# Kernel tuning notes

Hardware: AMD Instinct MI355X
Metric: run time of the kernel (lower is better)

The kernel has to match this reference:

```python
import jax, jax.numpy as jnp
import numpy as np

NUM_HEADS = 32
NUM_KV_HEADS = 8
HEAD_DIM = 128
HIDDEN = 4096
BASE = 10000.0


def setup_inputs() -> dict:
    key = jax.random.key(0)
    ks = jax.random.split(key, 9)
    bs, seq = 1, 2048
    x = jax.random.normal(ks[0], (bs, seq, HIDDEN), dtype=jnp.float32)
    position_ids = jnp.broadcast_to(jnp.arange(seq, dtype=jnp.int32), (bs, seq))
    s = 1.0 / np.sqrt(HIDDEN)
    wq = jax.random.normal(ks[1], (NUM_HEADS * HEAD_DIM, HIDDEN), dtype=jnp.float32) * s
    bq = jnp.zeros((NUM_HEADS * HEAD_DIM,), dtype=jnp.float32)
    wk = jax.random.normal(ks[2], (NUM_KV_HEADS * HEAD_DIM, HIDDEN), dtype=jnp.float32) * s
    bk = jnp.zeros((NUM_KV_HEADS * HEAD_DIM,), dtype=jnp.float32)
    wv = jax.random.normal(ks[3], (NUM_KV_HEADS * HEAD_DIM, HIDDEN), dtype=jnp.float32) * s
    bv = jnp.zeros((NUM_KV_HEADS * HEAD_DIM,), dtype=jnp.float32)
    wo = jax.random.normal(ks[4], (HIDDEN, NUM_HEADS * HEAD_DIM), dtype=jnp.float32) * s
    bo = jnp.zeros((HIDDEN,), dtype=jnp.float32)
    return {"x": x, "position_ids": position_ids, "wq": wq, "bq": bq,
            "wk": wk, "bk": bk, "wv": wv, "bv": bv, "wo": wo, "bo": bo}


def _rotate_half(t):
    h = t.shape[-1] // 2
    return jnp.concatenate([-t[..., h:], t[..., :h]], axis=-1)


def _rope_cos_sin(position_ids, dtype):
    # inv_freq: (head_dim/2,)
    inv_freq = 1.0 / (BASE ** (jnp.arange(0, HEAD_DIM, 2, dtype=jnp.float32) / HEAD_DIM))
    freqs = position_ids.astype(jnp.float32)[..., None] * inv_freq  # (bs, seq, hd/2)
    emb = jnp.concatenate([freqs, freqs], axis=-1)  # (bs, seq, hd)
    return jnp.cos(emb).astype(dtype), jnp.sin(emb).astype(dtype)


def reference(x, position_ids, wq, bq, wk, bk, wv, bv, wo, bo):
    bs, seq, _ = x.shape
    g = NUM_HEADS // NUM_KV_HEADS
    # projections -> (bs, heads, seq, head_dim)
    q = (x @ wq.T + bq).reshape(bs, seq, NUM_HEADS, HEAD_DIM).transpose(0, 2, 1, 3)
    k = (x @ wk.T + bk).reshape(bs, seq, NUM_KV_HEADS, HEAD_DIM).transpose(0, 2, 1, 3)
    v = (x @ wv.T + bv).reshape(bs, seq, NUM_KV_HEADS, HEAD_DIM).transpose(0, 2, 1, 3)
    cos, sin = _rope_cos_sin(position_ids, x.dtype)
    cos, sin = cos[:, None], sin[:, None]  # broadcast over heads
    q = q * cos + _rotate_half(q) * sin
    k = k * cos + _rotate_half(k) * sin
    # grouped attention without expanding kv (same math as repeat_kv)
    qg = q.reshape(bs, NUM_KV_HEADS, g, seq, HEAD_DIM)
    scores = jnp.einsum('bhgqd,bhkd->bhgqk', qg, k) / jnp.sqrt(
        jnp.asarray(HEAD_DIM, dtype=jnp.float32)).astype(x.dtype)
    probs = jax.nn.softmax(scores.astype(jnp.float32), axis=-1).astype(x.dtype)
    out = jnp.einsum('bhgqk,bhkd->bhgqd', probs, v)  # (bs, kvh, g, seq, hd)
    out = out.reshape(bs, NUM_HEADS, seq, HEAD_DIM).transpose(0, 2, 1, 3)
    out = out.reshape(bs, seq, NUM_HEADS * HEAD_DIM)
    return out @ wo.T + bo
```

## Files before the change

kernel.cpp:

```cpp
#include <hip/hip_runtime.h>
#include <stdint.h>

typedef unsigned short u16;
typedef unsigned long long u64;
typedef __attribute__((ext_vector_type(8))) short s8v;
typedef __attribute__((ext_vector_type(4))) float f4v;

#define MFMA(a, b, c) __builtin_amdgcn_mfma_f32_16x16x32_bf16((a), (b), (c), 0, 0, 0)

__device__ __forceinline__ u16 f2b(float f) {
  uint32_t x = __float_as_uint(f);
  x += 0x7fff + ((x >> 16) & 1);
  return (u16)(x >> 16);
}
__device__ __forceinline__ float b2f(u16 u) {
  return __uint_as_float(((uint32_t)u) << 16);
}

__device__ __forceinline__ void gll16(const void* g, void* l) {
  __builtin_amdgcn_global_load_lds((const __attribute__((address_space(1))) uint32_t*)g,
                                   (__attribute__((address_space(3))) uint32_t*)l, 16, 0, 0);
}
__device__ __forceinline__ void bar() { __builtin_amdgcn_s_barrier(); }

__global__ void cvt_all(const float* __restrict__ x, const float* __restrict__ wq,
                        const float* __restrict__ wk, const float* __restrict__ wv,
                        const float* __restrict__ wo,
                        u16* __restrict__ xb, u16* __restrict__ wqkv, u16* __restrict__ wob) {
  int i = blockIdx.x * 256 + threadIdx.x;
  const float* s; u16* d; size_t off;
  if      (i < 1048576) { s = x;  d = xb;   off = (size_t)i; }
  else if (i < 3145728) { s = wq; d = wqkv; off = (size_t)(i - 1048576); }
  else if (i < 3670016) { s = wk; d = wqkv + (size_t)16777216; off = (size_t)(i - 3145728); }
  else if (i < 4194304) { s = wv; d = wqkv + (size_t)20971520; off = (size_t)(i - 3670016); }
  else                  { s = wo; d = wob;  off = (size_t)(i - 4194304); }
  const float4* sp = (const float4*)(s + off * 8);
  float4 f0 = sp[0], f1 = sp[1];
  s8v o;
  o[0] = (short)f2b(f0.x); o[1] = (short)f2b(f0.y); o[2] = (short)f2b(f0.z); o[3] = (short)f2b(f0.w);
  o[4] = (short)f2b(f1.x); o[5] = (short)f2b(f1.y); o[6] = (short)f2b(f1.z); o[7] = (short)f2b(f1.w);
  *(s8v*)(d + off * 8) = o;
}

template <int BM, int MODE>
__global__ __launch_bounds__(512, 2) void gemm8p(
    const u16* __restrict__ A, const u16* __restrict__ Bact,
    const float* __restrict__ bias,
    float* __restrict__ Cf, u16* __restrict__ Cq, u16* __restrict__ Ck, u16* __restrict__ Cv,
    int K) {
  extern __shared__ u16 smem[];
  constexpr int AO = BM * 64;
  constexpr int BE = 2 * BM * 64;
  constexpr int BO = BE + 16384;
  constexpr int MI = BM / 64;
  constexpr int NH = BM / 64;

  const int tid = threadIdx.x;
  const int l = tid & 63, wv = tid >> 6;
  const int wm = wv >> 2, wn = wv & 3;
  const int lr = l & 15, lg = l >> 4;
  const int swz = 16 * (lr & 7);
  const int wrow = wm * (BM / 2);

  const int nwg = gridDim.x;
  int bid = blockIdx.x;
  bid = (bid & 7) * (nwg >> 3) + (bid >> 3);
  const int NB = 8;
  const int m0 = (bid / NB) * BM, n0 = (bid % NB) * 256;

  const size_t K64 = (size_t)64 * K;

  const int sr = tid >> 3;
  const int sc = ((tid & 7) ^ (sr & 7)) * 8;
  const u16* gA = A + (size_t)(m0 + sr) * K + sc;
  const u16* gB = Bact + (size_t)(n0 + sr) * K + sc;

  auto STA = [&](int P, int h, int kt) {
    gll16(gA + (size_t)(h * 64) * K + (size_t)kt * 64,
          smem + (P ? AO : 0) + h * 4096 + tid * 8);
  };
  auto STB = [&](int P, int h, int kt) {
    const u16* g = gB + (size_t)(h * 128) * K + (size_t)kt * 64;
    u16* d = smem + (P ? BO : BE) + h * 8192 + tid * 8;
    gll16(g, d);
    gll16(g + K64, d + 4096);
  };

  const char* smc = (const char*)smem;
  s8v a[MI][2], b0[2][2], b1[2][2];
  auto LDA = [&](int P, int QR) {
#pragma unroll
    for (int mi = 0; mi < MI; ++mi)
#pragma unroll
      for (int kk = 0; kk < 2; ++kk)
        a[mi][kk] = *(const s8v*)(smc + (P ? AO * 2 : 0) +
            (wrow + QR * (BM / 4) + mi * 16 + lr) * 128 + ((kk * 64 + lg * 16) ^ swz));
  };
  auto LDB = [&](int P, int QC, s8v bb[2][2]) {
#pragma unroll
    for (int ni = 0; ni < 2; ++ni)
#pragma unroll
      for (int kk = 0; kk < 2; ++kk)
        bb[ni][kk] = *(const s8v*)(smc + (P ? BO * 2 : BE * 2) +
            (wn * 64 + QC * 32 + ni * 16 + lr) * 128 + ((kk * 64 + lg * 16) ^ swz));
  };

  f4v acc[BM / 32][4];
#pragma unroll
  for (int i = 0; i < BM / 32; ++i)
#pragma unroll
    for (int j = 0; j < 4; ++j) acc[i][j] = {0.f, 0.f, 0.f, 0.f};

#define PHMF(QR, QC, B)                                                        \
  __builtin_amdgcn_s_setprio(1);                                               \
  _Pragma("unroll") for (int mi = 0; mi < MI; ++mi)                            \
    _Pragma("unroll") for (int ni = 0; ni < 2; ++ni)                           \
      _Pragma("unroll") for (int kk = 0; kk < 2; ++kk)                         \
        acc[(QR) * MI + mi][(QC) * 2 + ni] =                                   \
            MFMA(a[mi][kk], B[ni][kk], acc[(QR) * MI + mi][(QC) * 2 + ni]);    \
  __builtin_amdgcn_s_setprio(0);

  STB(0, 0, 0); STB(0, 1, 0);
#pragma unroll
  for (int h = 0; h < NH; ++h) STA(0, h, 0);
  STB(1, 0, 1); STB(1, 1, 1);
  asm volatile("s_waitcnt vmcnt(4)" ::: "memory");
  bar();

  const int ITERS = K >> 7;
  for (int i = 0; i < ITERS; ++i) {
    const int kn = 2 * i + 2;
    const bool more = (i + 1 < ITERS);
    LDA(0, 0); LDB(0, 0, b0);
    STA(1, 0, 2 * i + 1);
    bar(); PHMF(0, 0, b0); bar();
    LDB(0, 1, b1);
    STA(1, 1, 2 * i + 1);
    bar(); PHMF(0, 1, b1); bar();
    LDA(0, 1);
    if constexpr (NH > 2) STA(1, 2, 2 * i + 1);
    if (more) STB(0, 0, kn);
    bar(); PHMF(1, 1, b1); bar();
    if (more) STB(0, 1, kn);
    bar(); PHMF(1, 0, b0);
    if (more) asm volatile("s_waitcnt vmcnt(4)" ::: "memory");
    else      asm volatile("s_waitcnt vmcnt(0)" ::: "memory");
    bar();
    LDA(1, 0); LDB(1, 0, b0);
    if (more) STA(0, 0, kn);
    bar(); PHMF(0, 0, b0); bar();
    LDB(1, 1, b1);
    if (more) STA(0, 1, kn);
    bar(); PHMF(0, 1, b1); bar();
    LDA(1, 1);
    if (more) {
      if constexpr (NH > 2) STA(0, 2, kn);
      STB(1, 0, 2 * i + 3);
    }
    bar(); PHMF(1, 1, b1); bar();
    if (more) STB(1, 1, 2 * i + 3);
    bar(); PHMF(1, 0, b0);
    asm volatile("s_waitcnt vmcnt(4)" ::: "memory");
    bar();
  }
#undef PHMF

  bar();

  if constexpr (MODE == 2) {
#pragma unroll
    for (int fi = 0; fi < BM / 32; ++fi) {
      const int f0 = m0 + wrow + fi * 16;
      if (f0 >= 5120) {
#pragma unroll
        for (int fj = 0; fj < 4; ++fj)
#pragma unroll
          for (int r = 0; r < 4; ++r) {
            const int f = f0 + lg * 4 + r;
            const int tok = n0 + wn * 64 + fj * 16 + lr;
            Cv[(size_t)(f - 5120) * 2048 + tok] = f2b(acc[fi][fj][r] + bias[f]);
          }
      }
    }
    if (m0 + wrow < 5120) {
      u16* buf = smem + wv * 3328;
#pragma unroll
      for (int c = 0; c < 2; ++c) {
#pragma unroll
        for (int fj2 = 0; fj2 < 2; ++fj2) {
          const int fj = 2 * c + fj2;
          const int tl = fj2 * 16 + lr;
#pragma unroll
          for (int fi = 0; fi < BM / 32; ++fi) {
            const int f0 = m0 + wrow + fi * 16;
            if (f0 < 5120) {
#pragma unroll
              for (int r = 0; r < 4; ++r) {
                const int fl = fi * 16 + lg * 4 + r;
                buf[tl * 104 + fl] = f2b(acc[fi][fj][r] + bias[m0 + wrow + fl]);
              }
            }
          }
        }
        asm volatile("s_waitcnt lgkmcnt(0)" ::: "memory");
        const int row = l >> 1, half = l & 1;
        const int tok = n0 + wn * 64 + c * 32 + row;
#pragma unroll
        for (int i2 = 0; i2 < 6; ++i2) {
          const int flc = (2 * i2 + half) * 8;
          const int f = m0 + wrow + flc;
          if (f < 4096)
            *(s8v*)(Cq + (size_t)tok * 4096 + f) = *(const s8v*)(buf + row * 104 + flc);
          else if (f < 5120)
            *(s8v*)(Ck + (size_t)tok * 1024 + (f - 4096)) = *(const s8v*)(buf + row * 104 + flc);
        }
        asm volatile("s_waitcnt lgkmcnt(0)" ::: "memory");
      }
    }
  } else {
    float* buf = (float*)smem + wv * 1088;
#pragma unroll
    for (int c = 0; c < 4; ++c) {
#pragma unroll
      for (int fi = 0; fi < BM / 32; ++fi)
#pragma unroll
        for (int r = 0; r < 4; ++r) {
          const int fl = fi * 16 + lg * 4 + r;
          buf[lr * 68 + fl] = acc[fi][c][r] + bias[m0 + wrow + fl];
        }
      asm volatile("s_waitcnt lgkmcnt(0)" ::: "memory");
      const int row = l >> 2, q4 = l & 3;
      const int tok = n0 + wn * 64 + c * 16 + row;
      float* g = Cf + (size_t)tok * 4096 + m0 + wrow + q4 * 16;
      const float* src = buf + row * 68 + q4 * 16;
#pragma unroll
      for (int i2 = 0; i2 < 4; ++i2)
        *(f4v*)(g + i2 * 4) = *(const f4v*)(src + i2 * 4);
      asm volatile("s_waitcnt lgkmcnt(0)" ::: "memory");
    }
  }
}

__global__ void rope_kernel(u16* __restrict__ q, u16* __restrict__ k, const int* __restrict__ pos) {
  int i = blockIdx.x * 256 + threadIdx.x;
  const int NQ = 2048 * 32 * 64;
  const int NK = 2048 * 8 * 64;
  u16* buf;
  int m, d, stride, h;
  if (i < NQ) { buf = q; m = i >> 11; h = (i >> 6) & 31; d = i & 63; stride = 4096; }
  else {
    i -= NQ; if (i >= NK) return;
    buf = k; m = i >> 9; h = (i >> 6) & 7; d = i & 63; stride = 1024;
  }
  size_t base = (size_t)m * stride + h * 128 + d;
  float a = b2f(buf[base]), b = b2f(buf[base + 64]);
  float p = (float)pos[m];
  float ang = p * exp2f(-0.20762050593045952f * (float)d);
  float s, c;
  sincosf(ang, &s, &c);
  buf[base]      = f2b(a * c - b * s);
  buf[base + 64] = f2b(b * c + a * s);
}

__global__ __launch_bounds__(512, 4) void attn_kernel(const u16* __restrict__ Q, const u16* __restrict__ Kb,
                                                      const u16* __restrict__ Vt, u16* __restrict__ Ao) {
  __shared__ __align__(16) u16 Ks[64 * 128];
  __shared__ __align__(16) u16 Vs[128 * 64];
  __shared__ __align__(16) u16 Ps[8][16 * 64];
  const int tid = threadIdx.x;
  const int l = tid & 63, wv = tid >> 6;
  const int lr = l & 15, lg = l >> 4;
  const int head = blockIdx.x >> 4, qt = blockIdx.x & 15;
  const int kh = head >> 2;
  const int qrow = qt * 128 + wv * 16 + lr;

  s8v qf[4];
#pragma unroll
  for (int s = 0; s < 4; ++s)
    qf[s] = *(const s8v*)&Q[(size_t)qrow * 4096 + head * 128 + s * 32 + lg * 8];

  f4v zero = {0.f, 0.f, 0.f, 0.f};
  f4v ao[8];
#pragma unroll
  for (int tt = 0; tt < 8; ++tt) ao[tt] = zero;
  float mrun = -1e30f, lrun = 0.f;

  const int ki0 = tid, ki1 = tid + 512;
  const int kr0 = ki0 >> 4, kc0 = (ki0 & 15) ^ (kr0 & 7);
  const int kr1 = ki1 >> 4, kc1 = (ki1 & 15) ^ (kr1 & 7);
  const int vr0 = ki0 >> 3, vc0 = (ki0 & 7) ^ (vr0 & 7);
  const int vr1 = ki1 >> 3, vc1 = (ki1 & 7) ^ (vr1 & 7);
  const u16* Kg = Kb + kh * 128;
  const u16* Vg = Vt + (size_t)(kh * 128) * 2048;
  const u16* kp0 = Kg + (size_t)kr0 * 1024 + kc0 * 8;
  const u16* kp1 = Kg + (size_t)kr1 * 1024 + kc1 * 8;
  const u16* vp0 = Vg + (size_t)vr0 * 2048 + vc0 * 8;
  const u16* vp1 = Vg + (size_t)vr1 * 2048 + vc1 * 8;

  char* KsB = (char*)Ks;
  char* VsB = (char*)Vs;
  char* PwB = (char*)Ps[wv];
  const int swz = 16 * (lr & 7);
  const float C2 = 0.12753102f;

  for (int t = 0; t < 2048; t += 64) {
    __syncthreads();
    gll16(kp0 + (size_t)t * 1024, KsB + ki0 * 16);
    gll16(kp1 + (size_t)t * 1024, KsB + ki1 * 16);
    gll16(vp0 + t,                VsB + ki0 * 16);
    gll16(vp1 + t,                VsB + ki1 * 16);
    __syncthreads();

    f4v c[4];
#pragma unroll
    for (int j = 0; j < 4; ++j) c[j] = zero;
#pragma unroll
    for (int s = 0; s < 4; ++s) {
#pragma unroll
      for (int j = 0; j < 4; ++j) {
        s8v kf = *(const s8v*)(KsB + (16 * j + lr) * 256 + (((4 * s + lg) * 16) ^ swz));
        c[j] = MFMA(kf, qf[s], c[j]);
      }
    }

    float mx = fmaxf(fmaxf(c[0][0], c[0][1]), fmaxf(c[0][2], c[0][3]));
#pragma unroll
    for (int j = 1; j < 4; ++j)
      mx = fmaxf(mx, fmaxf(fmaxf(c[j][0], c[j][1]), fmaxf(c[j][2], c[j][3])));
    mx = fmaxf(mx, __shfl_xor(mx, 16));
    mx = fmaxf(mx, __shfl_xor(mx, 32));
    float m2x = mx * C2;

    if (!__all(m2x - mrun <= 8.f)) {
      float mnew = fmaxf(mrun, m2x);
      float alpha = __builtin_amdgcn_exp2f(mrun - mnew);
      float ar[4];
#pragma unroll
      for (int r = 0; r < 4; ++r) ar[r] = __shfl(alpha, 4 * lg + r);
#pragma unroll
      for (int tt = 0; tt < 8; ++tt)
#pragma unroll
        for (int r = 0; r < 4; ++r) ao[tt][r] *= ar[r];
      lrun *= alpha;
      mrun = mnew;
    }

    float rs = 0.f;
#pragma unroll
    for (int j = 0; j < 4; ++j) {
      float p0 = __builtin_amdgcn_exp2f(__builtin_fmaf(c[j][0], C2, -mrun));
      float p1 = __builtin_amdgcn_exp2f(__builtin_fmaf(c[j][1], C2, -mrun));
      float p2 = __builtin_amdgcn_exp2f(__builtin_fmaf(c[j][2], C2, -mrun));
      float p3 = __builtin_amdgcn_exp2f(__builtin_fmaf(c[j][3], C2, -mrun));
      rs += (p0 + p1) + (p2 + p3);
      uint32_t lo = (uint32_t)f2b(p0) | ((uint32_t)f2b(p1) << 16);
      uint32_t hi = (uint32_t)f2b(p2) | ((uint32_t)f2b(p3) << 16);
      u64 pak = (u64)lo | ((u64)hi << 32);
      *(u64*)(PwB + lr * 128 + ((32 * j + 8 * lg) ^ swz)) = pak;
    }
    rs += __shfl_xor(rs, 16);
    rs += __shfl_xor(rs, 32);
    lrun += rs;

#pragma unroll
    for (int h = 0; h < 2; ++h) {
      s8v pf = *(const s8v*)(PwB + lr * 128 + ((64 * h + 16 * lg) ^ swz));
#pragma unroll
      for (int tt = 0; tt < 8; ++tt) {
        s8v vf = *(const s8v*)(VsB + (16 * tt + lr) * 128 + (((4 * h + lg) * 16) ^ swz));
        ao[tt] = MFMA(pf, vf, ao[tt]);
      }
    }
  }

  float inv = 1.f / lrun;
  float ir[4];
#pragma unroll
  for (int r = 0; r < 4; ++r) ir[r] = __shfl(inv, 4 * lg + r);
#pragma unroll
  for (int tt = 0; tt < 8; ++tt)
#pragma unroll
    for (int r = 0; r < 4; ++r)
      Ao[(size_t)(qt * 128 + wv * 16 + 4 * lg + r) * 4096 + head * 128 + 16 * tt + lr] =
          f2b(ao[tt][r] * ir[r]);
}

extern "C" void kernel_launch(void* const* d_in, const int* in_sizes, int n_in,
                              void* d_out, int out_size, void* d_ws, size_t ws_size,
                              hipStream_t stream) {
  const float* x  = (const float*)d_in[0];
  const int*   pos = (const int*)d_in[1];
  const float* wq = (const float*)d_in[2];
  const float* bq = (const float*)d_in[3];
  const float* wk = (const float*)d_in[4];
  const float* bk = (const float*)d_in[5];
  const float* wv = (const float*)d_in[6];
  const float* bv = (const float*)d_in[7];
  const float* wo = (const float*)d_in[8];
  const float* bo = (const float*)d_in[9];
  float* out = (float*)d_out;

  char* ws = (char*)d_ws;
  u16* xb   = (u16*)(ws + 0);
  u16* wqkv = (u16*)(ws + 16777216);
  u16* wob  = (u16*)(ws + 67108864);
  u16* qb   = (u16*)(ws + 100663296);
  u16* kb   = (u16*)(ws + 117440512);
  u16* vT   = (u16*)(ws + 121634816);
  u16* ab   = (u16*)(ws + 125829120);
  float* bqkv = (float*)(ws + 142606336);

  hipMemcpyAsync(bqkv,        bq, 4096 * sizeof(float), hipMemcpyDeviceToDevice, stream);
  hipMemcpyAsync(bqkv + 4096, bk, 1024 * sizeof(float), hipMemcpyDeviceToDevice, stream);
  hipMemcpyAsync(bqkv + 5120, bv, 1024 * sizeof(float), hipMemcpyDeviceToDevice, stream);

  cvt_all<<<24576, 256, 0, stream>>>(x, wq, wk, wv, wo, xb, wqkv, wob);

  gemm8p<192, 2><<<256, 512, 114688, stream>>>(wqkv, xb, bqkv,
                                               nullptr, qb, kb, vT, 4096);
  rope_kernel<<<(2048 * 32 * 64 + 2048 * 8 * 64) / 256, 256, 0, stream>>>(qb, kb, pos);
  attn_kernel<<<512, 512, 0, stream>>>(qb, kb, vT, ab);
  gemm8p<128, 0><<<256, 512, 98304, stream>>>(wob, ab, bo,
                                              out, nullptr, nullptr, nullptr, 4096);
}
```

Measured before the change: 326.1 us.

## Double-buffer K/V tiles in attention and merge GEMM MFMA phases

The attention kernel now keeps two LDS buffers for K and V. It issues the global-to-LDS loads for the next 64-key tile before computing on the current one, and uses a single barrier per iteration, so memory latency overlaps with the QK and PV MFMAs. In the projection GEMM main loop, pairs of compute phases are merged: both B fragments and both A stores are issued up front, then two MFMA phases run under one raised-priority region, which halves the barrier count. The MODE 2 epilogue gains extra barriers so all waves hit the same number of barriers. The larger LDS footprint in attention (about 80KB per block) may reduce blocks per CU, and the merged GEMM phases keep more fragments live in registers.

Measured after the change: 327.5 us. Within noise of the previous version (+0.4%).

```diff
diff --git a/kernel.cpp b/kernel.cpp
--- a/kernel.cpp
+++ b/kernel.cpp
@@ -112,13 +112,11 @@
     for (int j = 0; j < 4; ++j) acc[i][j] = {0.f, 0.f, 0.f, 0.f};
 
 #define PHMF(QR, QC, B)                                                        \
-  __builtin_amdgcn_s_setprio(1);                                               \
   _Pragma("unroll") for (int mi = 0; mi < MI; ++mi)                            \
     _Pragma("unroll") for (int ni = 0; ni < 2; ++ni)                           \
       _Pragma("unroll") for (int kk = 0; kk < 2; ++kk)                         \
         acc[(QR) * MI + mi][(QC) * 2 + ni] =                                   \
-            MFMA(a[mi][kk], B[ni][kk], acc[(QR) * MI + mi][(QC) * 2 + ni]);    \
-  __builtin_amdgcn_s_setprio(0);
+            MFMA(a[mi][kk], B[ni][kk], acc[(QR) * MI + mi][(QC) * 2 + ni]);
 
   STB(0, 0, 0); STB(0, 1, 0);
 #pragma unroll
@@ -131,35 +129,39 @@
   for (int i = 0; i < ITERS; ++i) {
     const int kn = 2 * i + 2;
     const bool more = (i + 1 < ITERS);
-    LDA(0, 0); LDB(0, 0, b0);
-    STA(1, 0, 2 * i + 1);
-    bar(); PHMF(0, 0, b0); bar();
-    LDB(0, 1, b1);
-    STA(1, 1, 2 * i + 1);
-    bar(); PHMF(0, 1, b1); bar();
+    LDA(0, 0); LDB(0, 0, b0); LDB(0, 1, b1);
+    STA(1, 0, 2 * i + 1); STA(1, 1, 2 * i + 1);
+    bar();
+    __builtin_amdgcn_s_setprio(1);
+    PHMF(0, 0, b0); PHMF(0, 1, b1);
+    __builtin_amdgcn_s_setprio(0);
+    bar();
     LDA(0, 1);
     if constexpr (NH > 2) STA(1, 2, 2 * i + 1);
-    if (more) STB(0, 0, kn);
-    bar(); PHMF(1, 1, b1); bar();
-    if (more) STB(0, 1, kn);
-    bar(); PHMF(1, 0, b0);
+    if (more) { STB(0, 0, kn); STB(0, 1, kn); }
+    bar();
+    __builtin_amdgcn_s_setprio(1);
+    PHMF(1, 1, b1); PHMF(1, 0, b0);
+    __builtin_amdgcn_s_setprio(0);
     if (more) asm volatile("s_waitcnt vmcnt(4)" ::: "memory");
     else      asm volatile("s_waitcnt vmcnt(0)" ::: "memory");
     bar();
-    LDA(1, 0); LDB(1, 0, b0);
-    if (more) STA(0, 0, kn);
-    bar(); PHMF(0, 0, b0); bar();
-    LDB(1, 1, b1);
-    if (more) STA(0, 1, kn);
-    bar(); PHMF(0, 1, b1); bar();
+    LDA(1, 0); LDB(1, 0, b0); LDB(1, 1, b1);
+    if (more) { STA(0, 0, kn); STA(0, 1, kn); }
+    bar();
+    __builtin_amdgcn_s_setprio(1);
+    PHMF(0, 0, b0); PHMF(0, 1, b1);
+    __builtin_amdgcn_s_setprio(0);
+    bar();
     LDA(1, 1);
     if (more) {
       if constexpr (NH > 2) STA(0, 2, kn);
-      STB(1, 0, 2 * i + 3);
-    }
-    bar(); PHMF(1, 1, b1); bar();
-    if (more) STB(1, 1, 2 * i + 3);
-    bar(); PHMF(1, 0, b0);
+      STB(1, 0, 2 * i + 3); STB(1, 1, 2 * i + 3);
+    }
+    bar();
+    __builtin_amdgcn_s_setprio(1);
+    PHMF(1, 1, b1); PHMF(1, 0, b0);
+    __builtin_amdgcn_s_setprio(0);
     asm volatile("s_waitcnt vmcnt(4)" ::: "memory");
     bar();
   }
@@ -215,7 +217,10 @@
             *(s8v*)(Ck + (size_t)tok * 1024 + (f - 4096)) = *(const s8v*)(buf + row * 104 + flc);
         }
         asm volatile("s_waitcnt lgkmcnt(0)" ::: "memory");
+        bar();
       }
+    } else {
+      bar(); bar();
     }
   } else {
     float* buf = (float*)smem + wv * 1088;
@@ -264,8 +269,8 @@
 
 __global__ __launch_bounds__(512, 4) void attn_kernel(const u16* __restrict__ Q, const u16* __restrict__ Kb,
                                                       const u16* __restrict__ Vt, u16* __restrict__ Ao) {
-  __shared__ __align__(16) u16 Ks[64 * 128];
-  __shared__ __align__(16) u16 Vs[128 * 64];
+  __shared__ __align__(16) u16 Ks[2][64 * 128];
+  __shared__ __align__(16) u16 Vs[2][128 * 64];
   __shared__ __align__(16) u16 Ps[8][16 * 64];
   const int tid = threadIdx.x;
   const int l = tid & 63, wv = tid >> 6;
@@ -297,19 +302,25 @@
   const u16* vp0 = Vg + (size_t)vr0 * 2048 + vc0 * 8;
   const u16* vp1 = Vg + (size_t)vr1 * 2048 + vc1 * 8;
 
-  char* KsB = (char*)Ks;
-  char* VsB = (char*)Vs;
+  auto stage = [&](int b, int t) {
+    gll16(kp0 + (size_t)t * 1024, (char*)Ks[b] + ki0 * 16);
+    gll16(kp1 + (size_t)t * 1024, (char*)Ks[b] + ki1 * 16);
+    gll16(vp0 + t,                (char*)Vs[b] + ki0 * 16);
+    gll16(vp1 + t,                (char*)Vs[b] + ki1 * 16);
+  };
+
   char* PwB = (char*)Ps[wv];
   const int swz = 16 * (lr & 7);
   const float C2 = 0.12753102f;
 
+  stage(0, 0);
+  __syncthreads();
+
   for (int t = 0; t < 2048; t += 64) {
-    __syncthreads();
-    gll16(kp0 + (size_t)t * 1024, KsB + ki0 * 16);
-    gll16(kp1 + (size_t)t * 1024, KsB + ki1 * 16);
-    gll16(vp0 + t,                VsB + ki0 * 16);
-    gll16(vp1 + t,                VsB + ki1 * 16);
-    __syncthreads();
+    const int cur = (t >> 6) & 1;
+    if (t + 64 < 2048) stage(cur ^ 1, t + 64);
+    const char* KsB = (const char*)Ks[cur];
+    const char* VsB = (const char*)Vs[cur];
 
     f4v c[4];
 #pragma unroll
@@ -371,6 +382,8 @@
         ao[tt] = MFMA(pf, vf, ao[tt]);
       }
     }
+
+    __syncthreads();
   }
 
   float inv = 1.f / lrun;
```
